# Performance work log

Measured on AMD Instinct MI355X. Metric: run time of the kernel, lower is better.

Reference implementation:

```python
import jax, jax.numpy as jnp
import numpy as np
import math

N_HEADS = 16
ROPE_THETA = 10000.0
NEG_INF = -1e30


def setup_inputs() -> dict:
    key = jax.random.key(0)
    k1, k2, k3, k4 = jax.random.split(key, 4)
    B, S, D = 2, 2048, 2048
    x = jax.random.normal(k1, (B, S, D), dtype=jnp.float32)
    qkv = 0.01 * jax.random.normal(k2, (2 * D, D), dtype=jnp.float32)
    H = N_HEADS
    dh = D // H
    nope = dh // 2
    rope = dh // 2
    wk = 0.01 * jax.random.normal(k3, (H * nope + rope, D), dtype=jnp.float32)
    wo = 0.01 * jax.random.normal(k4, (D, D), dtype=jnp.float32)
    return {"x": x, "qkv": qkv, "wk": wk, "wo": wo}


def _rope_cos_sin(S, dh, rope_dim, dtype):
    # freqs over full dh as in the torch module, then sliced to rope_dim//2 and tiled x2
    freqs = 1.0 / (ROPE_THETA ** (jnp.arange(0, dh, 2).astype(jnp.float32) / dh))
    emb = jnp.arange(S, dtype=jnp.float32)[:, None] * freqs[None, :]  # [S, dh//2]
    cos = jnp.tile(jnp.cos(emb)[:, : rope_dim // 2], (1, 2))[None, None]  # [1,1,S,rope]
    sin = jnp.tile(jnp.sin(emb)[:, : rope_dim // 2], (1, 2))[None, None]
    return cos.astype(dtype), sin.astype(dtype)


def _apply_rope(xq, cos, sin):
    x1, x2 = jnp.split(xq, 2, axis=-1)
    return xq * cos + jnp.concatenate([-x2, x1], axis=-1) * sin


def reference(x, qkv, wk, wo):
    B, S, D = x.shape
    H = N_HEADS
    dh = D // H
    nope = dh // 2
    rope = dh // 2

    QV = x @ qkv.T                              # [B,S,2D]
    Q, V = jnp.split(QV, 2, axis=-1)
    Q = Q.reshape(B, S, H, dh).transpose(0, 2, 1, 3)        # [B,H,S,dh]
    v_heads = V.reshape(B, S, H, dh).transpose(0, 2, 1, 3)  # [B,H,S,dh]
    Qn, Qr = Q[..., :nope], Q[..., nope:]

    K = x @ wk.T                                # [B,S,H*nope+rope]
    Kn = K[..., : H * nope].reshape(B, S, H, nope).transpose(0, 2, 1, 3)  # [B,H,S,nope]
    Kr = K[..., H * nope :].reshape(B, S, 1, rope).transpose(0, 2, 1, 3)  # [B,1,S,rope]

    cos, sin = _rope_cos_sin(S, dh, rope, x.dtype)
    Qr = _apply_rope(Qr, cos, sin)
    Kr = _apply_rope(Kr, cos, sin)

    q_heads = jnp.concatenate([Qn, Qr], axis=-1)                               # [B,H,S,dh]
    k_heads = jnp.concatenate([Kn, jnp.broadcast_to(Kr, (B, H, S, rope))], -1)  # [B,H,S,dh]

    scale = 1.0 / math.sqrt(dh)
    scores = jnp.einsum('bhqd,bhkd->bhqk', q_heads, k_heads) * scale
    mask = jnp.tril(jnp.ones((S, S), dtype=bool))
    scores = jnp.where(mask[None, None], scores, NEG_INF)
    attn = jax.nn.softmax(scores, axis=-1)
    out = jnp.einsum('bhqk,bhkd->bhqd', attn, v_heads)
    out = out.transpose(0, 2, 1, 3).reshape(B, S, D) @ wo.T
    return (out, k_heads, v_heads)
```

## Files before the change

kernel.cpp:

```cpp
#include <hip/hip_runtime.h>
#include <hip/hip_bf16.h>


typedef unsigned short u16;
typedef unsigned int u32;
typedef __bf16 bf16x8 __attribute__((ext_vector_type(8)));
typedef float f32x4 __attribute__((ext_vector_type(4)));
typedef float f32x16 __attribute__((ext_vector_type(16)));

__device__ __forceinline__ u16 f2bf(float x) {
  union { __hip_bfloat16 h; u16 u; } c;
  c.h = __float2bfloat16(x);
  return c.u;
}
__device__ __forceinline__ float bf2f(u16 u) {
  union { u32 u; float f; } c;
  c.u = ((u32)u) << 16;
  return c.f;
}
__device__ __forceinline__ u32 pack2(float a, float b) {
  return (u32)f2bf(a) | ((u32)f2bf(b) << 16);
}
__device__ __forceinline__ f32x4 mfma16(bf16x8 a, bf16x8 b, f32x4 c) {
  return __builtin_amdgcn_mfma_f32_16x16x32_bf16(a, b, c, 0, 0, 0);
}
__device__ __forceinline__ f32x16 mfma32(bf16x8 a, bf16x8 b, f32x16 c) {
  return __builtin_amdgcn_mfma_f32_32x32x16_bf16(a, b, c, 0, 0, 0);
}
__device__ __forceinline__ void gload_lds16(const void* g, void* l) {
  __builtin_amdgcn_global_load_lds((__attribute__((address_space(1))) void*)g,
                                   (__attribute__((address_space(3))) void*)l,
                                   16, 0, 0);
}

__global__ __launch_bounds__(256) void cast_all(const float4* __restrict__ x,
                                                const float4* __restrict__ qkv,
                                                const float* __restrict__ wk,
                                                const float4* __restrict__ wo,
                                                u16* __restrict__ x_bf,
                                                u16* __restrict__ wcomb,
                                                u16* __restrict__ wo_bf) {
  int i = blockIdx.x * blockDim.x + threadIdx.x;
  const float4* src;
  u16* dst;
  int j;
  if (i < 2097152) {
    src = x; dst = x_bf; j = i;
  } else if (i < 4194304) {
    src = qkv; dst = wcomb; j = i - 2097152;
  } else if (i < 4849664) {
    j = i - 4194304;
    int r = (j * 4) >> 11;
    u32 lo = 0, hi = 0;
    if (r < 1088) {
      float4 v = ((const float4*)wk)[j];
      lo = pack2(v.x, v.y);
      hi = pack2(v.z, v.w);
    }
    ((uint2*)(wcomb + 8388608))[j] = make_uint2(lo, hi);
    return;
  } else {
    src = wo; dst = wo_bf; j = i - 4849664;
  }
  float4 v = src[j];
  ((uint2*)dst)[j] = make_uint2(pack2(v.x, v.y), pack2(v.z, v.w));
}

__device__ __forceinline__ void cstore(u16* C, size_t i, float v) { C[i] = f2bf(v); }
__device__ __forceinline__ void cstore(float* C, size_t i, float v) { C[i] = v; }

template <typename CT, int BM, int BN>
__global__ __launch_bounds__(512, 2) void gemm256(const u16* __restrict__ A,
                                                  const u16* __restrict__ W,
                                                  CT* __restrict__ C,
                                                  int M, int N, int K) {
  constexpr int MI = BM / 64;
  constexpr int NI = BN / 128;
  constexpr int AH = BM * 64;
  constexpr int BH = BN * 64;
  constexpr int AL = BM / 128;
  constexpr int BL = BN / 128;
  constexpr int BOFF = 4 * AH;
  __shared__ char lds[BOFF + 4 * BH];
  const int tid = threadIdx.x;
  const int wid = tid >> 6, lane = tid & 63;
  const int lr = lane & 15, lg = lane >> 4;
  const int wr = wid >> 2, wc = wid & 3;
  const int xorv = (lr & 7) << 4;
  const int nwg = gridDim.x * gridDim.y;
  const int lin = blockIdx.y * gridDim.x + blockIdx.x;
  const int swz = (lin & 7) * (nwg >> 3) + (lin >> 3);
  const int m0 = (swz / gridDim.x) * BM;
  const int n0 = (swz % gridDim.x) * BN;
  const int nkt = K >> 6;

  f32x4 acc[2 * MI][2 * NI] = {};
  bf16x8 a[MI][2], b[2 * NI][2];

  const int o0 = tid * 16, o1 = 8192 + tid * 16;
  const int r0 = o0 >> 7, c0 = ((o0 & 127) ^ ((r0 & 7) << 4)) >> 1;
  const int r1 = o1 >> 7, c1 = ((o1 & 127) ^ ((r1 & 7) << 4)) >> 1;
  const u16* gA0[2] = {A + (size_t)(m0 + r0) * K + c0,
                       A + (size_t)(m0 + BM / 2 + r0) * K + c0};
  const u16* gA1[2] = {A + (size_t)(m0 + r1) * K + c1,
                       A + (size_t)(m0 + BM / 2 + r1) * K + c1};
  const u16* gB0[2] = {W + (size_t)(n0 + r0) * K + c0,
                       W + (size_t)(n0 + BN / 2 + r0) * K + c0};
  const u16* gB1[2] = {W + (size_t)(n0 + r1) * K + c1,
                       W + (size_t)(n0 + BN / 2 + r1) * K + c1};

  auto STAGEA = [&](int t, int h) {
    char* d_ = lds + (t & 1) * (2 * AH) + h * AH + wid * 1024;
    gload_lds16(gA0[h] + (size_t)t * 64, d_);
    if constexpr (AL == 2) gload_lds16(gA1[h] + (size_t)t * 64, d_ + 8192);
  };
  auto STAGEB = [&](int t, int h) {
    char* d_ = lds + BOFF + (t & 1) * (2 * BH) + h * BH + wid * 1024;
    gload_lds16(gB0[h] + (size_t)t * 64, d_);
    if constexpr (BL == 2) gload_lds16(gB1[h] + (size_t)t * 64, d_ + 8192);
  };
  auto WAITKEEP = [&]() {
    if constexpr (AL + BL == 4) asm volatile("s_waitcnt vmcnt(4)" ::: "memory");
    else asm volatile("s_waitcnt vmcnt(3)" ::: "memory");
  };

  STAGEA(0, 0); STAGEB(0, 0); STAGEA(0, 1); STAGEB(0, 1);
  if (nkt > 1) { STAGEA(1, 0); STAGEB(1, 0); }
  WAITKEEP();
  __builtin_amdgcn_s_barrier();

  for (int t = 0; t < nkt; ++t) {
    const char* Ab = lds + (t & 1) * (2 * AH);
    const char* Bb = lds + BOFF + (t & 1) * (2 * BH);
    const int arow = wr * (BM / 4), brow = wc * (BN / 8);
#pragma unroll
    for (int mi = 0; mi < MI; mi++)
#pragma unroll
      for (int ks = 0; ks < 2; ks++)
        a[mi][ks] = *(const bf16x8*)(Ab + (arow + mi * 16 + lr) * 128 + ((lg * 16 + ks * 64) ^ xorv));
#pragma unroll
    for (int ni = 0; ni < NI; ni++)
#pragma unroll
      for (int ks = 0; ks < 2; ks++)
        b[ni][ks] = *(const bf16x8*)(Bb + (brow + ni * 16 + lr) * 128 + ((lg * 16 + ks * 64) ^ xorv));
    if (t + 1 < nkt) STAGEA(t + 1, 1);
    __builtin_amdgcn_s_barrier();
    asm volatile("s_waitcnt lgkmcnt(0)" ::: "memory");
    __builtin_amdgcn_sched_barrier(0);
    __builtin_amdgcn_s_setprio(1);
#pragma unroll
    for (int mi = 0; mi < MI; mi++)
#pragma unroll
      for (int ni = 0; ni < NI; ni++)
#pragma unroll
        for (int ks = 0; ks < 2; ks++)
          acc[mi][ni] = mfma16(a[mi][ks], b[ni][ks], acc[mi][ni]);
    __builtin_amdgcn_s_setprio(0);
    __builtin_amdgcn_s_barrier();
#pragma unroll
    for (int ni = 0; ni < NI; ni++)
#pragma unroll
      for (int ks = 0; ks < 2; ks++)
        b[NI + ni][ks] = *(const bf16x8*)(Bb + BH + (brow + ni * 16 + lr) * 128 + ((lg * 16 + ks * 64) ^ xorv));
    if (t + 1 < nkt) STAGEB(t + 1, 1);
    __builtin_amdgcn_s_barrier();
    asm volatile("s_waitcnt lgkmcnt(0)" ::: "memory");
    __builtin_amdgcn_sched_barrier(0);
    __builtin_amdgcn_s_setprio(1);
#pragma unroll
    for (int mi = 0; mi < MI; mi++)
#pragma unroll
      for (int ni = 0; ni < NI; ni++)
#pragma unroll
        for (int ks = 0; ks < 2; ks++)
          acc[mi][NI + ni] = mfma16(a[mi][ks], b[NI + ni][ks], acc[mi][NI + ni]);
    __builtin_amdgcn_s_setprio(0);
    __builtin_amdgcn_s_barrier();
#pragma unroll
    for (int mi = 0; mi < MI; mi++)
#pragma unroll
      for (int ks = 0; ks < 2; ks++)
        a[mi][ks] = *(const bf16x8*)(Ab + AH + (arow + mi * 16 + lr) * 128 + ((lg * 16 + ks * 64) ^ xorv));
    if (t + 2 < nkt) STAGEA(t + 2, 0);
    __builtin_amdgcn_s_barrier();
    asm volatile("s_waitcnt lgkmcnt(0)" ::: "memory");
    __builtin_amdgcn_sched_barrier(0);
    __builtin_amdgcn_s_setprio(1);
#pragma unroll
    for (int mi = 0; mi < MI; mi++)
#pragma unroll
      for (int ni = 0; ni < NI; ni++)
#pragma unroll
        for (int ks = 0; ks < 2; ks++)
          acc[MI + mi][ni] = mfma16(a[mi][ks], b[ni][ks], acc[MI + mi][ni]);
    __builtin_amdgcn_s_setprio(0);
    __builtin_amdgcn_s_barrier();
    if (t + 2 < nkt) {
      STAGEB(t + 2, 0);
      WAITKEEP();
    } else if (t + 1 < nkt) {
      asm volatile("s_waitcnt vmcnt(0)" ::: "memory");
    }
    __builtin_amdgcn_s_barrier();
    asm volatile("s_waitcnt lgkmcnt(0)" ::: "memory");
    __builtin_amdgcn_sched_barrier(0);
    __builtin_amdgcn_s_setprio(1);
#pragma unroll
    for (int mi = 0; mi < MI; mi++)
#pragma unroll
      for (int ni = 0; ni < NI; ni++)
#pragma unroll
        for (int ks = 0; ks < 2; ks++)
          acc[MI + mi][NI + ni] = mfma16(a[mi][ks], b[NI + ni][ks], acc[MI + mi][NI + ni]);
    __builtin_amdgcn_s_setprio(0);
    __builtin_amdgcn_s_barrier();
  }

#pragma unroll
  for (int Mh = 0; Mh < 2; Mh++)
#pragma unroll
    for (int mi = 0; mi < MI; mi++) {
      int row = m0 + Mh * (BM / 2) + wr * (BM / 4) + mi * 16 + lg * 4;
#pragma unroll
      for (int Nh = 0; Nh < 2; Nh++)
#pragma unroll
        for (int ni = 0; ni < NI; ni++) {
          int col = n0 + Nh * (BN / 2) + wc * (BN / 8) + ni * 16 + lr;
#pragma unroll
          for (int r = 0; r < 4; r++)
            cstore(C, (size_t)(row + r) * N + col, acc[Mh * MI + mi][Nh * NI + ni][r]);
        }
    }
}

__global__ __launch_bounds__(256) void rope_scatter2(u16* __restrict__ QVK,
                                                     u16* __restrict__ kh,
                                                     float* __restrict__ k_out, int S) {
  const int row = blockIdx.x;
  const int b = row >> 11, s = row & 2047;
  const int tid = threadIdx.x;
  __shared__ float kr[64];
  const float LOG1E4_64 = 0.14391156511f;
  u16* qrow = QVK + (size_t)row * 5376;
  if (tid < 32) {
    float freq = __expf(-(float)tid * LOG1E4_64);
    float sn, c;
    __sincosf((float)s * freq, &sn, &c);
    float a = bf2f(qrow[5120 + tid]);
    float bb = bf2f(qrow[5152 + tid]);
    kr[tid] = a * c - bb * sn;
    kr[tid + 32] = bb * c + a * sn;
  }
  for (int idx = tid; idx < 512; idx += 256) {
    int h = idx >> 5, jj = idx & 31;
    float freq = __expf(-(float)jj * LOG1E4_64);
    float sn, c;
    __sincosf((float)s * freq, &sn, &c);
    u16* p1 = qrow + h * 128 + 64 + jj;
    u16* p2 = qrow + h * 128 + 96 + jj;
    float x1 = bf2f(*p1), x2 = bf2f(*p2);
    *p1 = f2bf(x1 * c - x2 * sn);
    *p2 = f2bf(x2 * c + x1 * sn);
  }
  __syncthreads();
  for (int idx = tid; idx < 2048; idx += 256) {
    int h = idx >> 7, d = idx & 127;
    float val = (d < 64) ? bf2f(qrow[4096 + h * 64 + d]) : kr[d - 64];
    size_t o = ((size_t)(b * 16 + h) * S + s) * 128 + d;
    kh[o] = f2bf(val);
    k_out[o] = val;
  }
}

__global__ __launch_bounds__(256) void v_scatter(const u16* __restrict__ QVK,
                                                 u16* __restrict__ vt,
                                                 float* __restrict__ v_out, int S) {
  const int blk = blockIdx.x;
  const int st = blk & 63;
  const int dt = (blk >> 6) & 3;
  const int bh = blk >> 8;
  const int b = bh >> 4, h = bh & 15;
  __shared__ u16 t[32][34];
  const int tx = threadIdx.x & 31, ty = threadIdx.x >> 5;
  const int s0 = st * 32, d0 = dt * 32;
#pragma unroll
  for (int i = 0; i < 4; i++) {
    int sl = ty + 8 * i;
    u16 u = QVK[(size_t)(b * S + s0 + sl) * 5376 + 2048 + h * 128 + d0 + tx];
    t[sl][tx] = u;
    v_out[((size_t)bh * S + s0 + sl) * 128 + d0 + tx] = bf2f(u);
  }
  __syncthreads();
#pragma unroll
  for (int i = 0; i < 4; i++) {
    int dl = ty + 8 * i;
    vt[((size_t)bh * 128 + d0 + dl) * S + s0 + tx] = t[tx][dl];
  }
}

__global__ __launch_bounds__(256) void flash_attn8(const u16* __restrict__ QVK,
                                                   const u16* __restrict__ Kh,
                                                   const u16* __restrict__ Vt,
                                                   u16* __restrict__ attn, int S) {
  __shared__ char lds[49664];
  const int tid = threadIdx.x, wid = tid >> 6, lane = tid & 63;
  const int bh = blockIdx.x & 31;
  const int qb = 15 - (int)(blockIdx.x >> 5);
  const int q0w = qb * 128 + wid * 32;
  const int b = bh >> 4, h = bh & 15;
  const int r32 = lane & 31, hh = lane >> 5;
  const u16* Qb = QVK + (size_t)b * S * 5376 + h * 128;
  const u16* Kb = Kh + (size_t)bh * S * 128;
  const u16* Vb = Vt + (size_t)bh * 128 * S;
  const int qg = q0w + r32;
  const int xr = (r32 & 7) << 4;
  char* const Pc = lds + 49152 + wid * 128;

  const u16 *srcK[4], *srcV[4];
#pragma unroll
  for (int i = 0; i < 4; i++) {
    int o = i * 4096 + tid * 16;
    int rK = o >> 8, cbK = (o & 255) ^ ((rK & 7) << 4);
    srcK[i] = Kb + rK * 128 + (cbK >> 1);
    int dV = o >> 7, kbV = (o & 127) ^ ((dV & 7) << 4);
    srcV[i] = Vb + (size_t)dV * S + (kbV >> 1);
  }

  bf16x8 qf[8];
#pragma unroll
  for (int f = 0; f < 8; f++)
    qf[f] = *(const bf16x8*)(Qb + (size_t)qg * 5376 + f * 16 + hh * 8);

  f32x16 acc[4] = {};
  float m = -INFINITY, l = 0.f;
  const float sc = 0.08838834764831845f;
  const int ktiles = 2 * qb + 2;

  uint4 vreg[4];
#pragma unroll
  for (int i = 0; i < 4; i++) vreg[i] = *(const uint4*)srcV[i];
#pragma unroll
  for (int i = 0; i < 4; i++)
    gload_lds16(srcK[i], lds + i * 4096 + wid * 1024);
  asm volatile("s_waitcnt vmcnt(4)" ::: "memory");
#pragma unroll
  for (int i = 0; i < 4; i++)
    *(uint4*)(lds + 32768 + i * 4096 + tid * 16) = vreg[i];
  asm volatile("s_waitcnt lgkmcnt(0)" ::: "memory");
  __builtin_amdgcn_s_barrier();

  for (int kt = 0; kt < ktiles; ++kt) {
    const char* Kt = lds + (kt & 1) * 16384;
    const char* Vl = lds + 32768;
    const bool more = (kt + 1 < ktiles);
    if (more) {
#pragma unroll
      for (int i = 0; i < 4; i++)
        vreg[i] = *(const uint4*)(srcV[i] + (size_t)(kt + 1) * 64);
#pragma unroll
      for (int i = 0; i < 4; i++)
        gload_lds16(srcK[i] + (size_t)(kt + 1) * 8192,
                    lds + (((kt & 1) ^ 1) << 14) + i * 4096 + wid * 1024);
      asm volatile("s_waitcnt vmcnt(8)" ::: "memory");
    } else {
      asm volatile("s_waitcnt vmcnt(0)" ::: "memory");
    }
    __builtin_amdgcn_s_barrier();

    const int kbg = kt * 64;
    const bool active = (kbg <= q0w + 31);
    if (active) {
      u32 u[16];
      f32x16 s[2] = {};
      __builtin_amdgcn_s_setprio(1);
#pragma unroll
      for (int kg = 0; kg < 2; kg++) {
        const char* Kq = Kt + (kg * 32 + r32) * 256;
#pragma unroll
        for (int f = 0; f < 8; f++) {
          bf16x8 kf = *(const bf16x8*)(Kq + ((f * 32 + hh * 16) ^ xr));
          s[kg] = mfma32(kf, qf[f], s[kg]);
        }
      }
      __builtin_amdgcn_s_setprio(0);
      const bool maskt = (kbg + 63 > q0w);
      if (maskt) {
#pragma unroll
        for (int kg = 0; kg < 2; kg++)
#pragma unroll
          for (int r = 0; r < 16; r++)
            if (kbg + kg * 32 + (r & 3) + 8 * (r >> 2) + 4 * hh > qg)
              s[kg][r] = -1e30f;
      }
      float tm = s[0][0];
#pragma unroll
      for (int r = 1; r < 16; r++) tm = fmaxf(tm, s[0][r]);
#pragma unroll
      for (int r = 0; r < 16; r++) tm = fmaxf(tm, s[1][r]);
      tm = fmaxf(tm, __shfl_xor(tm, 32));
      if (!__all(tm <= m + 64.0f)) {
        float mnew = fmaxf(m, tm);
        float corr = __expf((m - mnew) * sc);
        m = mnew;
        l *= corr;
        if (lane < 32) *(float*)(Pc + r32 * 4) = corr;
        asm volatile("s_waitcnt lgkmcnt(0)" ::: "memory");
        __builtin_amdgcn_sched_barrier(0);
        f32x4 c0 = *(const f32x4*)(Pc + (4 * hh) * 4);
        f32x4 c1 = *(const f32x4*)(Pc + (8 + 4 * hh) * 4);
        f32x4 c2 = *(const f32x4*)(Pc + (16 + 4 * hh) * 4);
        f32x4 c3 = *(const f32x4*)(Pc + (24 + 4 * hh) * 4);
#pragma unroll
        for (int dg = 0; dg < 4; dg++)
#pragma unroll
          for (int r = 0; r < 16; r++) {
            float cr = (r >> 2) == 0 ? c0[r & 3]
                     : (r >> 2) == 1 ? c1[r & 3]
                     : (r >> 2) == 2 ? c2[r & 3] : c3[r & 3];
            acc[dg][r] *= cr;
          }
      }
      const float nms = -m * sc;
      float ts = 0.f;
#pragma unroll
      for (int kg = 0; kg < 2; kg++)
#pragma unroll
        for (int r = 0; r < 16; r++) {
          float pv = __expf(fmaf(s[kg][r], sc, nms));
          s[kg][r] = pv;
          ts += pv;
        }
      ts += __shfl_xor(ts, 32);
      l += ts;
#pragma unroll
      for (int kg = 0; kg < 2; kg++)
#pragma unroll
        for (int i = 0; i < 8; i++)
          u[kg * 8 + i] = pack2(s[kg][2 * i], s[kg][2 * i + 1]);

      __builtin_amdgcn_s_setprio(1);
#pragma unroll
      for (int dg = 0; dg < 4; dg++) {
        const char* Vq = Vl + (dg * 32 + r32) * 128;
#pragma unroll
        for (int ss = 0; ss < 4; ss++) {
          uint2 vlo = *(const uint2*)(Vq + ((ss * 32 + 8 * hh) ^ xr));
          uint2 vhi = *(const uint2*)(Vq + ((ss * 32 + 16 + 8 * hh) ^ xr));
          union { u32 w[4]; bf16x8 v; } vb, pa;
          vb.w[0] = vlo.x; vb.w[1] = vlo.y; vb.w[2] = vhi.x; vb.w[3] = vhi.y;
          pa.w[0] = u[ss * 4 + 0];
          pa.w[1] = u[ss * 4 + 1];
          pa.w[2] = u[ss * 4 + 2];
          pa.w[3] = u[ss * 4 + 3];
          acc[dg] = mfma32(pa.v, vb.v, acc[dg]);
        }
      }
      __builtin_amdgcn_s_setprio(0);
    }

    __builtin_amdgcn_s_barrier();
    if (more) {
      asm volatile("s_waitcnt vmcnt(4)" ::: "memory");
#pragma unroll
      for (int i = 0; i < 4; i++)
        *(uint4*)(lds + 32768 + i * 4096 + tid * 16) = vreg[i];
      asm volatile("s_waitcnt lgkmcnt(0)" ::: "memory");
    }
    __builtin_amdgcn_s_barrier();
  }

  float linv = 1.0f / l;
  if (lane < 32) *(float*)(Pc + r32 * 4) = linv;
  asm volatile("s_waitcnt lgkmcnt(0)" ::: "memory");
  __builtin_amdgcn_sched_barrier(0);
  f32x4 l0 = *(const f32x4*)(Pc + (4 * hh) * 4);
  f32x4 l1 = *(const f32x4*)(Pc + (8 + 4 * hh) * 4);
  f32x4 l2 = *(const f32x4*)(Pc + (16 + 4 * hh) * 4);
  f32x4 l3 = *(const f32x4*)(Pc + (24 + 4 * hh) * 4);
  u16* ab = attn + (size_t)(b * S + q0w) * 2048 + h * 128;
#pragma unroll
  for (int dg = 0; dg < 4; dg++)
#pragma unroll
    for (int r = 0; r < 16; r++) {
      int rowl = (r & 3) + 8 * (r >> 2) + 4 * hh;
      float li = (r >> 2) == 0 ? l0[r & 3]
               : (r >> 2) == 1 ? l1[r & 3]
               : (r >> 2) == 2 ? l2[r & 3] : l3[r & 3];
      ab[(size_t)rowl * 2048 + dg * 32 + r32] = f2bf(acc[dg][r] * li);
    }
}

extern "C" void kernel_launch(void* const* d_in, const int* in_sizes, int n_in,
                              void* d_out, int out_size, void* d_ws, size_t ws_size,
                              hipStream_t stream) {
  (void)in_sizes; (void)n_in; (void)out_size; (void)ws_size;
  const int S = 2048;
  const float* x = (const float*)d_in[0];
  const float* qkv = (const float*)d_in[1];
  const float* wk = (const float*)d_in[2];
  const float* wo = (const float*)d_in[3];
  float* out = (float*)d_out;
  float* k_out = out + (size_t)8388608;
  float* v_out = out + (size_t)16777216;

  char* ws = (char*)d_ws;
  u16* x_bf  = (u16*)(ws + 0);
  u16* wcomb = (u16*)(ws + 16777216);
  u16* wo_bf = (u16*)(ws + 38797312);
  u16* qvk   = (u16*)(ws + 47185920);
  u16* vt_bf = (u16*)(ws + 91226112);
  u16* attn_bf = x_bf;
  u16* k_bf = wcomb;

  cast_all<<<23040, 256, 0, stream>>>((const float4*)x, (const float4*)qkv, wk,
                                      (const float4*)wo, x_bf, wcomb, wo_bf);

  gemm256<u16, 256, 256><<<dim3(16, 16), 512, 0, stream>>>(x_bf, wcomb, qvk,
                                                           4096, 5376, 2048);
  gemm256<u16, 256, 128><<<dim3(10, 16), 512, 0, stream>>>(
      x_bf, wcomb + (size_t)4096 * 2048, qvk + 4096, 4096, 5376, 2048);
  rope_scatter2<<<4096, 256, 0, stream>>>(qvk, k_bf, k_out, S);
  v_scatter<<<8192, 256, 0, stream>>>(qvk, vt_bf, v_out, S);
  flash_attn8<<<512, 256, 0, stream>>>(qvk, k_bf, vt_bf, attn_bf, S);
  gemm256<float, 128, 256><<<dim3(8, 32), 512, 0, stream>>>(attn_bf, wo_bf, out,
                                                            4096, 2048, 2048);
}
```

Before: 306.1 us.

## Double-buffer V tile in LDS via direct global-to-LDS loads

The attention kernel now double-buffers the V tile in LDS alongside K. Both are loaded with asynchronous global-to-LDS loads, replacing the register staging and the extra barrier pair used to copy V into LDS at the end of each iteration. The max and sum reductions over the score registers are also changed from serial chains to tree reductions to shorten the dependency chains. LDS use grows to about 66 KB per block, which may reduce occupancy.

```diff
diff --git a/kernel.cpp b/kernel.cpp
--- a/kernel.cpp
+++ b/kernel.cpp
@@ -298,11 +298,11 @@
   }
 }
 
-__global__ __launch_bounds__(256) void flash_attn8(const u16* __restrict__ QVK,
-                                                   const u16* __restrict__ Kh,
-                                                   const u16* __restrict__ Vt,
-                                                   u16* __restrict__ attn, int S) {
-  __shared__ char lds[49664];
+__global__ __launch_bounds__(256) void flash_attn10(const u16* __restrict__ QVK,
+                                                    const u16* __restrict__ Kh,
+                                                    const u16* __restrict__ Vt,
+                                                    u16* __restrict__ attn, int S) {
+  __shared__ char lds[66048];
   const int tid = threadIdx.x, wid = tid >> 6, lane = tid & 63;
   const int bh = blockIdx.x & 31;
   const int qb = 15 - (int)(blockIdx.x >> 5);
@@ -314,7 +314,7 @@
   const u16* Vb = Vt + (size_t)bh * 128 * S;
   const int qg = q0w + r32;
   const int xr = (r32 & 7) << 4;
-  char* const Pc = lds + 49152 + wid * 128;
+  char* const Pc = lds + 65536 + wid * 128;
 
   const u16 *srcK[4], *srcV[4];
 #pragma unroll
@@ -336,37 +336,33 @@
   const float sc = 0.08838834764831845f;
   const int ktiles = 2 * qb + 2;
 
-  uint4 vreg[4];
-#pragma unroll
-  for (int i = 0; i < 4; i++) vreg[i] = *(const uint4*)srcV[i];
-#pragma unroll
-  for (int i = 0; i < 4; i++)
+#pragma unroll
+  for (int i = 0; i < 4; i++) {
     gload_lds16(srcK[i], lds + i * 4096 + wid * 1024);
-  asm volatile("s_waitcnt vmcnt(4)" ::: "memory");
-#pragma unroll
-  for (int i = 0; i < 4; i++)
-    *(uint4*)(lds + 32768 + i * 4096 + tid * 16) = vreg[i];
-  asm volatile("s_waitcnt lgkmcnt(0)" ::: "memory");
+    gload_lds16(srcV[i], lds + 32768 + i * 4096 + wid * 1024);
+  }
+  asm volatile("s_waitcnt vmcnt(0)" ::: "memory");
   __builtin_amdgcn_s_barrier();
 
   for (int kt = 0; kt < ktiles; ++kt) {
-    const char* Kt = lds + (kt & 1) * 16384;
-    const char* Vl = lds + 32768;
     const bool more = (kt + 1 < ktiles);
     if (more) {
-#pragma unroll
-      for (int i = 0; i < 4; i++)
-        vreg[i] = *(const uint4*)(srcV[i] + (size_t)(kt + 1) * 64);
-#pragma unroll
-      for (int i = 0; i < 4; i++)
+      const int dst = ((kt + 1) & 1) << 14;
+#pragma unroll
+      for (int i = 0; i < 4; i++) {
         gload_lds16(srcK[i] + (size_t)(kt + 1) * 8192,
-                    lds + (((kt & 1) ^ 1) << 14) + i * 4096 + wid * 1024);
+                    lds + dst + i * 4096 + wid * 1024);
+        gload_lds16(srcV[i] + (size_t)(kt + 1) * 64,
+                    lds + 32768 + dst + i * 4096 + wid * 1024);
+      }
       asm volatile("s_waitcnt vmcnt(8)" ::: "memory");
     } else {
       asm volatile("s_waitcnt vmcnt(0)" ::: "memory");
     }
     __builtin_amdgcn_s_barrier();
 
+    const char* Kt = lds + (kt & 1) * 16384;
+    const char* Vl = lds + 32768 + (kt & 1) * 16384;
     const int kbg = kt * 64;
     const bool active = (kbg <= q0w + 31);
     if (active) {
@@ -392,11 +388,15 @@
             if (kbg + kg * 32 + (r & 3) + 8 * (r >> 2) + 4 * hh > qg)
               s[kg][r] = -1e30f;
       }
-      float tm = s[0][0];
-#pragma unroll
-      for (int r = 1; r < 16; r++) tm = fmaxf(tm, s[0][r]);
-#pragma unroll
-      for (int r = 0; r < 16; r++) tm = fmaxf(tm, s[1][r]);
+      float mx[16];
+#pragma unroll
+      for (int r = 0; r < 16; r++) mx[r] = fmaxf(s[0][r], s[1][r]);
+#pragma unroll
+      for (int st = 8; st > 0; st >>= 1)
+#pragma unroll
+        for (int r = 0; r < 8; r++)
+          if (r < st) mx[r] = fmaxf(mx[r], mx[r + st]);
+      float tm = mx[0];
       tm = fmaxf(tm, __shfl_xor(tm, 32));
       if (!__all(tm <= m + 64.0f)) {
         float mnew = fmaxf(m, tm);
@@ -421,15 +421,20 @@
           }
       }
       const float nms = -m * sc;
-      float ts = 0.f;
+      float sm[16];
 #pragma unroll
       for (int kg = 0; kg < 2; kg++)
 #pragma unroll
-        for (int r = 0; r < 16; r++) {
-          float pv = __expf(fmaf(s[kg][r], sc, nms));
-          s[kg][r] = pv;
-          ts += pv;
-        }
+        for (int r = 0; r < 16; r++)
+          s[kg][r] = __expf(fmaf(s[kg][r], sc, nms));
+#pragma unroll
+      for (int r = 0; r < 16; r++) sm[r] = s[0][r] + s[1][r];
+#pragma unroll
+      for (int st = 8; st > 0; st >>= 1)
+#pragma unroll
+        for (int r = 0; r < 8; r++)
+          if (r < st) sm[r] = sm[r] + sm[r + st];
+      float ts = sm[0];
       ts += __shfl_xor(ts, 32);
       l += ts;
 #pragma unroll
@@ -457,15 +462,6 @@
       }
       __builtin_amdgcn_s_setprio(0);
     }
-
-    __builtin_amdgcn_s_barrier();
-    if (more) {
-      asm volatile("s_waitcnt vmcnt(4)" ::: "memory");
-#pragma unroll
-      for (int i = 0; i < 4; i++)
-        *(uint4*)(lds + 32768 + i * 4096 + tid * 16) = vreg[i];
-      asm volatile("s_waitcnt lgkmcnt(0)" ::: "memory");
-    }
     __builtin_amdgcn_s_barrier();
   }
 
@@ -521,7 +517,7 @@
       x_bf, wcomb + (size_t)4096 * 2048, qvk + 4096, 4096, 5376, 2048);
   rope_scatter2<<<4096, 256, 0, stream>>>(qvk, k_bf, k_out, S);
   v_scatter<<<8192, 256, 0, stream>>>(qvk, vt_bf, v_out, S);
-  flash_attn8<<<512, 256, 0, stream>>>(qvk, k_bf, vt_bf, attn_bf, S);
+  flash_attn10<<<512, 256, 0, stream>>>(qvk, k_bf, vt_bf, attn_bf, S);
   gemm256<float, 128, 256><<<dim3(8, 32), 512, 0, stream>>>(attn_bf, wo_bf, out,
                                                             4096, 2048, 2048);
 }
```

Result: faster. 271.1 us (-11.4%).
